# Kernel optimization log

Measured on AMD Instinct MI355X. Metric: run time of the kernel, lower is better.

Reference implementation:

```python
import jax, jax.numpy as jnp
import numpy as np

RADII = (0.4, 0.8, 1.2)
SIGMA2 = 2.0 * 0.2 ** 2   # Gaussian shell-density bandwidth
ALPHA = 0.3               # keras LeakyReLU default
EPS = 1e-3                # keras BatchNormalization default epsilon


def _n_coeffs(L):
    return sum((2 * l + 1) ** 2 for l in range(L + 1))


def _pullback_idx(L):
    # flat index of Wigner block entry (m, n=0) for each SH coeff (l, m)
    idx, off = [], 0
    for l in range(L + 1):
        d = 2 * l + 1
        idx += [off + m * d + l for m in range(d)]
        off += d * d
    return np.asarray(idx, dtype=np.int32)


def setup_inputs() -> dict:
    key = jax.random.key(0)
    ks = jax.random.split(key, 20)
    B, N, Q, S = 64, 2048, 1024, 512
    T = [_n_coeffs(l) for l in (5, 4, 3)]  # 286, 165, 84
    f32 = jnp.float32

    def nrm(k, shape, scale=1.0):
        return jax.random.normal(ks[k], shape, dtype=f32) * scale

    dirs = nrm(1, (3, S, 3))
    dirs = dirs / jnp.linalg.norm(dirs, axis=-1, keepdims=True)
    z = lambda n: jnp.zeros((n,), f32)
    o = lambda n: jnp.ones((n,), f32)
    return {
        "x": nrm(0, (B, N, 3)),
        "shell_dirs": dirs,                                   # [3, 512, 3]
        "A_sh": nrm(2, (36, S), 1.0 / np.sqrt(S)),            # SH projection (l_max=5)
        "D_eval0": nrm(3, (Q, T[0]), 1.0 / np.sqrt(T[0])),    # Wigner eval bases
        "D_eval1": nrm(4, (Q, T[1]), 1.0 / np.sqrt(T[1])),
        "D_eval2": nrm(5, (Q, T[2]), 1.0 / np.sqrt(T[2])),
        "D_coef1": nrm(6, (T[1], Q), 1.0 / np.sqrt(Q)),       # Wigner coeff (projection) bases
        "D_coef2": nrm(7, (T[2], Q), 1.0 / np.sqrt(Q)),
        "D_coef_last": nrm(8, (T[2], Q), 1.0 / np.sqrt(Q)),
        "W0": nrm(9, (3, 16), 1.0 / np.sqrt(3)), "b0": z(16),
        "W1": nrm(10, (16, 32), 0.25), "b1": z(32),
        "W2": nrm(11, (32, 64), 1.0 / np.sqrt(32)), "b2": z(64),
        "g0": o(16), "be0": z(16),
        "g1": o(32), "be1": z(32),
        "g2": o(64), "be2": z(64),
        "Wfc1": nrm(12, (256, 512), 1.0 / 16.0), "bfc1": z(512),
        "gfc1": o(512), "befc1": z(512),
        "Wfc2": nrm(13, (512, 256), 1.0 / np.sqrt(512)), "bfc2": z(256),
        "gfc2": o(256), "befc2": z(256),
        "Wout": nrm(14, (256, 40), 1.0 / 16.0), "bout": z(40),
    }


def _bn(y, g, b, axes):
    m = jnp.mean(y, axis=axes, keepdims=True)
    v = jnp.var(y, axis=axes, keepdims=True)
    return (y - m) * jax.lax.rsqrt(v + EPS) * g + b


def reference(x, shell_dirs, A_sh, D_eval0, D_eval1, D_eval2,
              D_coef1, D_coef2, D_coef_last,
              W0, b0, W1, b1, W2, b2,
              g0, be0, g1, be1, g2, be2,
              Wfc1, bfc1, gfc1, befc1, Wfc2, bfc2, gfc2, befc2,
              Wout, bout):
    B = x.shape[0]
    # --- sphere_shell_embedding: Gaussian shell density -> SH coeffs per shell ---
    xn2 = jnp.sum(x * x, -1)[..., None]                 # [B,N,1]
    sh = []
    for i, r in enumerate(RADII):
        c = r * shell_dirs[i]                           # [S,3]
        d2 = xn2 + jnp.sum(c * c, -1) - 2.0 * (x @ c.T)  # [B,N,S]
        f = jnp.mean(jnp.exp(-d2 / SIGMA2), axis=1)      # [B,S]
        sh.append(f @ A_sh.T)                            # [B,36]
    sh = jnp.stack(sh, axis=-1)                          # [B,36,3] shells as channels
    # --- S2_to_SO3_pullback: Y_lm -> D^l_{m,0} column of Wigner blocks ---
    idx = jnp.asarray(_pullback_idx(5))
    y = jnp.zeros((B, 286, 3), sh.dtype).at[:, idx, :].set(sh)
    # --- layer 0: SO3Conv (per-coeff channel mix) + WignerEval + BN + LReLU + WignerCoeffs ---
    y = jnp.einsum('btc,cu->btu', y, W0) + b0
    y = jnp.einsum('qt,btu->bqu', D_eval0, y)            # [B,1024,16]
    y = jax.nn.leaky_relu(_bn(y, g0, be0, (0, 1)), ALPHA)
    y = jnp.einsum('tq,bqu->btu', D_coef1, y)            # [B,165,16]
    # --- layer 1 ---
    y = jnp.einsum('btc,cu->btu', y, W1) + b1
    y = jnp.einsum('qt,btu->bqu', D_eval1, y)            # [B,1024,32]
    y = jax.nn.leaky_relu(_bn(y, g1, be1, (0, 1)), ALPHA)
    y = jnp.einsum('tq,bqu->btu', D_coef2, y)            # [B,84,32]
    # --- layer 2 ---
    y = jnp.einsum('btc,cu->btu', y, W2) + b2
    y = jnp.einsum('qt,btu->bqu', D_eval2, y)            # [B,1024,64]
    y = jax.nn.leaky_relu(_bn(y, g2, be2, (0, 1)), ALPHA)
    y = jnp.einsum('tq,bqu->btu', D_coef_last, y)        # [B,84,64]
    # --- degree-wise norms (rotation-invariant pooling), l_max=3 blocks ---
    offs, sizes = (0, 1, 10, 35), (1, 9, 25, 49)
    feats = jnp.concatenate(
        [jnp.linalg.norm(y[:, o:o + s, :], axis=1, keepdims=True)
         for o, s in zip(offs, sizes)], axis=1)          # [B,4,64]
    h = feats.reshape(B, -1)                             # [B,256]
    # --- MLP head (dropout = identity at inference) ---
    h = jax.nn.relu(_bn(h @ Wfc1 + bfc1, gfc1, befc1, (0,)))
    h = jax.nn.relu(_bn(h @ Wfc2 + bfc2, gfc2, befc2, (0,)))
    return jax.nn.softmax(h @ Wout + bout, axis=-1)
```

## Files before the change

### kernel.cpp

```cpp
#include <hip/hip_runtime.h>
#include <hip/hip_bf16.h>

#define BB 64
#define NN 2048
#define QQ 1024
#define SS 512
#define NCH 16
#define PREPB 609
#define QKN3 4

__device__ const int PIDX[36] = {
    0, 2, 5, 8, 12, 17, 22, 27, 32, 38, 45, 52, 59, 66, 73, 80,
    88, 97, 106, 115, 124, 133, 142, 151, 160,
    170, 181, 192, 203, 214, 225, 236, 247, 258, 269, 280};

__global__ __launch_bounds__(256) void k_preshell(
    const float* __restrict__ De0, const float* __restrict__ De1, const float* __restrict__ De2,
    float* __restrict__ Dg0t, float* __restrict__ rs0,
    float* __restrict__ Det1, float* __restrict__ Det2,
    float* __restrict__ stats,
    const float* __restrict__ x, const float* __restrict__ dirs, float* __restrict__ pbuf) {
    __shared__ float tile[32][33];
    __shared__ float4 lx[NN / NCH];
    int blk = blockIdx.x, tid = threadIdx.x;
    if (blk < PREPB) {
        int r = tid >> 5, c = tid & 31;
        if (blk < 192) {
            int tq = blk & 31, tt = blk >> 5;
            int q0 = tq * 32, t0 = tt * 32;
            for (int rr = r; rr < 32; rr += 8) {
                int t = t0 + c;
                tile[rr][c] = (t < 165) ? De1[(q0 + rr) * 165 + t] : 0.f;
            }
            __syncthreads();
            for (int rr = r; rr < 32; rr += 8) {
                int t = t0 + rr;
                if (t < 165) Det1[t * QQ + q0 + c] = tile[c][rr];
            }
        } else if (blk < 288) {
            int i = blk - 192;
            int tq = i & 31, tt = i >> 5;
            int q0 = tq * 32, t0 = tt * 32;
            for (int rr = r; rr < 32; rr += 8) {
                int t = t0 + c;
                tile[rr][c] = (t < 84) ? De2[(q0 + rr) * 84 + t] : 0.f;
            }
            __syncthreads();
            for (int rr = r; rr < 32; rr += 8) {
                int t = t0 + rr;
                if (t < 84) Det2[t * QQ + q0 + c] = tile[c][rr];
            }
        } else if (blk < 352) {
            int i = blk - 288;
            int tq = i & 31, tj = i >> 5;
            int q0 = tq * 32, j0 = tj * 32;
            for (int rr = r; rr < 32; rr += 8) {
                int j = j0 + c;
                tile[rr][c] = (j < 36) ? De0[(q0 + rr) * 286 + PIDX[j]] : 0.f;
            }
            __syncthreads();
            for (int rr = r; rr < 32; rr += 8) {
                int j = j0 + rr;
                if (j < 36) Dg0t[j * QQ + q0 + c] = tile[c][rr];
            }
        } else if (blk < 608) {
            int w = tid >> 6, lane = tid & 63;
            int q = (blk - 352) * 4 + w;
            float s = 0.f;
#pragma unroll
            for (int p = 0; p < 5; p++) {
                int idx = lane + p * 64;
                if (idx < 286) s += De0[q * 286 + idx];
            }
#pragma unroll
            for (int o = 32; o > 0; o >>= 1) s += __shfl_xor(s, o, 64);
            if (lane == 0) rs0[q] = s;
        } else {
            if (tid < 224) stats[tid] = 0.f;
        }
        return;
    }
    int idx = blk - PREPB;
    int b = idx & 63, zc = idx >> 6;
    const float KL = 18.033688011112042f;
    const float* xb = x + ((size_t)b * NN + zc * (NN / NCH)) * 3;
    for (int n = tid; n < NN / NCH; n += 256) {
        float X = xb[n * 3 + 0];
        float Y = xb[n * 3 + 1];
        float Z = xb[n * 3 + 2];
        lx[n] = make_float4(X, Y, Z, -KL * (X * X + Y * Y + Z * Z));
    }
    __syncthreads();
    float cxs[3][2], cys[3][2], czs[3][2], bas[3][2];
#pragma unroll
    for (int i = 0; i < 3; i++) {
        float r = (i == 0) ? 0.4f : ((i == 1) ? 0.8f : 1.2f);
#pragma unroll
        for (int h = 0; h < 2; h++) {
            int s = tid + h * 256;
            float cx = r * dirs[(i * SS + s) * 3 + 0];
            float cy = r * dirs[(i * SS + s) * 3 + 1];
            float cz = r * dirs[(i * SS + s) * 3 + 2];
            bas[i][h] = -KL * (cx * cx + cy * cy + cz * cz);
            cxs[i][h] = 2.f * KL * cx;
            cys[i][h] = 2.f * KL * cy;
            czs[i][h] = 2.f * KL * cz;
        }
    }
    float acc[3][2];
#pragma unroll
    for (int i = 0; i < 3; i++) { acc[i][0] = 0.f; acc[i][1] = 0.f; }
#pragma unroll 4
    for (int n = 0; n < NN / NCH; n++) {
        float4 p = lx[n];
#pragma unroll
        for (int i = 0; i < 3; i++)
#pragma unroll
            for (int h = 0; h < 2; h++)
                acc[i][h] += __builtin_amdgcn_exp2f(
                    fmaf(cxs[i][h], p.x, fmaf(cys[i][h], p.y, fmaf(czs[i][h], p.z, p.w + bas[i][h]))));
    }
#pragma unroll
    for (int i = 0; i < 3; i++) {
        float* o = pbuf + ((size_t)(zc * 3 + i) * BB + b) * SS;
        o[tid] = acc[i][0];
        o[tid + 256] = acc[i][1];
    }
}

__global__ __launch_bounds__(256) void k_eval0(const float* __restrict__ pbuf,
                                               const float* __restrict__ A_sh,
                                               const float* __restrict__ W0,
                                               const float* __restrict__ b0,
                                               const float* __restrict__ Dg0t,
                                               const float* __restrict__ rs0,
                                               float* __restrict__ yq, float* __restrict__ stats) {
    __shared__ float lf[3][SS];
    __shared__ float lsh[36][3];
    __shared__ float llm[576];
    __shared__ float lred[4][32];
    int qc = blockIdx.x, b = blockIdx.y, tid = threadIdx.x;
    for (int i = tid; i < 3 * SS; i += 256) {
        int c = i / SS, s = i % SS;
        float v = 0.f;
#pragma unroll
        for (int zc = 0; zc < NCH; zc++) v += pbuf[((size_t)(zc * 3 + c) * BB + b) * SS + s];
        lf[c][s] = v * (1.0f / NN);
    }
    __syncthreads();
    int w = tid >> 6, lane = tid & 63;
    for (int p = w; p < 108; p += 4) {
        int j = p / 3, c = p % 3;
        const float* As = A_sh + j * SS;
        float a = 0.f;
#pragma unroll
        for (int k = 0; k < 8; k++) a = fmaf(lf[c][lane + 64 * k], As[lane + 64 * k], a);
#pragma unroll
        for (int o = 32; o > 0; o >>= 1) a += __shfl_xor(a, o, 64);
        if (lane == 0) lsh[j][c] = a;
    }
    __syncthreads();
    for (int i = tid; i < 576; i += 256) {
        int j = i >> 4, u = i & 15;
        float m = 0.f;
#pragma unroll
        for (int c = 0; c < 3; c++) m = fmaf(lsh[j][c], W0[c * 16 + u], m);
        llm[i] = m;
    }
    __syncthreads();
    int q = qc * 256 + tid;
    float acc[16];
#pragma unroll
    for (int u = 0; u < 16; u++) acc[u] = 0.f;
#pragma unroll 4
    for (int j = 0; j < 36; j++) {
        float d = Dg0t[j * QQ + q];
#pragma unroll
        for (int u = 0; u < 16; u++) acc[u] = fmaf(d, llm[j * 16 + u], acc[u]);
    }
    float rb = rs0[q];
#pragma unroll
    for (int u = 0; u < 16; u++) acc[u] = fmaf(b0[u], rb, acc[u]);
#pragma unroll
    for (int u = 0; u < 16; u++) yq[((size_t)b * 16 + u) * QQ + q] = acc[u];
#pragma unroll
    for (int u = 0; u < 16; u++) {
        float v = acc[u], v2 = acc[u] * acc[u];
#pragma unroll
        for (int o = 32; o > 0; o >>= 1) {
            v += __shfl_xor(v, o, 64);
            v2 += __shfl_xor(v2, o, 64);
        }
        if (lane == 0) { lred[w][u] = v; lred[w][16 + u] = v2; }
    }
    __syncthreads();
    if (tid < 32) atomicAdd(&stats[tid], lred[0][tid] + lred[1][tid] + lred[2][tid] + lred[3][tid]);
}

template <int TT, int UU, int QKN>
__global__ __launch_bounds__(256) void k_coefG(const float* __restrict__ yq,
                                               const float* __restrict__ Dc,
                                               const float* __restrict__ stats,
                                               const float* __restrict__ g,
                                               const float* __restrict__ be,
                                               float* __restrict__ part) {
    constexpr int KC = QQ / QKN;
    __shared__ float lA[32][68];
    __shared__ float lB[32][68];
    __shared__ float lsu[UU], ltu[UU];
    int mt = blockIdx.x, nt = blockIdx.y, qk = blockIdx.z, tid = threadIdx.x;
    int m0 = mt * 64, n0 = nt * 64, k0 = qk * KC;
    if (tid < UU) {
        const float inv = 1.0f / (BB * QQ);
        float mm = stats[tid] * inv;
        float var = stats[UU + tid] * inv - mm * mm;
        float s = g[tid] * rsqrtf(fmaxf(var, 0.f) + 1e-3f);
        lsu[tid] = s;
        ltu[tid] = be[tid] - mm * s;
    }
    __syncthreads();
    int r = tid >> 2;
    int f = (tid & 3) * 4;
    bool mok = (m0 + r) < TT;
    const float* arow = Dc + (size_t)(mok ? (m0 + r) : 0) * QQ;
    const float* brow = yq + (size_t)(n0 + r) * QQ;
    float su = lsu[(n0 + r) % UU], tu = ltu[(n0 + r) % UU];
    int tg = tid >> 4, ug = tid & 15;
    float acc[4][4];
#pragma unroll
    for (int i = 0; i < 4; i++)
#pragma unroll
        for (int j = 0; j < 4; j++) acc[i][j] = 0.f;
    for (int kb = 0; kb < KC; kb += 32) {
        int kg = k0 + kb;
#pragma unroll
        for (int p = 0; p < 2; p++) {
            int ko = f + p * 16;
            float4 a4 = make_float4(0.f, 0.f, 0.f, 0.f);
            if (mok) a4 = *(const float4*)(arow + kg + ko);
            float4 b4 = *(const float4*)(brow + kg + ko);
#pragma unroll
            for (int i = 0; i < 4; i++) {
                float v = fmaf((&b4.x)[i], su, tu);
                lA[ko + i][r] = (&a4.x)[i];
                lB[ko + i][r] = (v > 0.f) ? v : 0.3f * v;
            }
        }
        __syncthreads();
#pragma unroll 2
        for (int kk = 0; kk < 32; kk++) {
            float4 a4 = *(const float4*)&lA[kk][tg * 4];
            float4 b4 = *(const float4*)&lB[kk][ug * 4];
#pragma unroll
            for (int i = 0; i < 4; i++) {
                float av = (&a4.x)[i];
                acc[i][0] = fmaf(av, b4.x, acc[i][0]);
                acc[i][1] = fmaf(av, b4.y, acc[i][1]);
                acc[i][2] = fmaf(av, b4.z, acc[i][2]);
                acc[i][3] = fmaf(av, b4.w, acc[i][3]);
            }
        }
        __syncthreads();
    }
    int n = n0 + ug * 4;
    int b = n / UU, u0 = n % UU;
#pragma unroll
    for (int i = 0; i < 4; i++) {
        int t = m0 + tg * 4 + i;
        if (t < TT)
            *(float4*)&part[(((size_t)qk * BB + b) * TT + t) * UU + u0] =
                make_float4(acc[i][0], acc[i][1], acc[i][2], acc[i][3]);
    }
}

template <int TT, int CC, int UU, int QKN>
__global__ __launch_bounds__(256) void k_eval(const float* __restrict__ part,
                                              const float* __restrict__ W, const float* __restrict__ bias,
                                              const float* __restrict__ Det,
                                              float* __restrict__ yq, float* __restrict__ stats) {
    __shared__ float lyt[TT * CC];
    __shared__ float lym[TT * 16];
    __shared__ float lred[4][32];
    int qc = blockIdx.x, b = blockIdx.y, uz = blockIdx.z * 16, tid = threadIdx.x;
    for (int i = tid; i < TT * CC; i += 256) {
        float v = 0.f;
#pragma unroll
        for (int k = 0; k < QKN; k++) v += part[(size_t)k * (BB * TT * CC) + (size_t)b * TT * CC + i];
        lyt[i] = v;
    }
    __syncthreads();
    for (int e = tid; e < TT * 16; e += 256) {
        int t = e >> 4, ul = e & 15, u = uz + ul;
        float m = bias[u];
#pragma unroll
        for (int c = 0; c < CC; c++) m = fmaf(lyt[t * CC + c], W[c * UU + u], m);
        lym[e] = m;
    }
    __syncthreads();
    int q = qc * 256 + tid;
    float acc[16];
#pragma unroll
    for (int u = 0; u < 16; u++) acc[u] = 0.f;
#pragma unroll 4
    for (int t = 0; t < TT; t++) {
        float d = Det[t * QQ + q];
#pragma unroll
        for (int u = 0; u < 16; u++) acc[u] = fmaf(d, lym[t * 16 + u], acc[u]);
    }
#pragma unroll
    for (int u = 0; u < 16; u++) yq[((size_t)b * UU + uz + u) * QQ + q] = acc[u];
    int lane = tid & 63, w = tid >> 6;
#pragma unroll
    for (int u = 0; u < 16; u++) {
        float v = acc[u], v2 = acc[u] * acc[u];
#pragma unroll
        for (int o = 32; o > 0; o >>= 1) {
            v += __shfl_xor(v, o, 64);
            v2 += __shfl_xor(v2, o, 64);
        }
        if (lane == 0) { lred[w][u] = v; lred[w][16 + u] = v2; }
    }
    __syncthreads();
    if (tid < 32) {
        float s = lred[0][tid] + lred[1][tid] + lred[2][tid] + lred[3][tid];
        int idx = (tid < 16) ? (uz + tid) : (UU + uz + tid - 16);
        atomicAdd(&stats[idx], s);
    }
}

__global__ __launch_bounds__(256) void k_norms(const float* __restrict__ part, float* __restrict__ ht0) {
    __shared__ float ly[84 * 64];
    int b = blockIdx.x, tid = threadIdx.x;
    for (int i = tid; i < 84 * 64; i += 256) {
        float v = 0.f;
#pragma unroll
        for (int k = 0; k < QKN3; k++) v += part[(size_t)k * (BB * 84 * 64) + b * (84 * 64) + i];
        ly[i] = v;
    }
    __syncthreads();
    int blk = tid >> 6, u = tid & 63;
    const int offs[4] = {0, 1, 10, 35};
    const int ends[4] = {1, 10, 35, 84};
    float a = 0.f;
    for (int t = offs[blk]; t < ends[blk]; t++) {
        float v = ly[t * 64 + u];
        a = fmaf(v, v, a);
    }
    ht0[(blk * 64 + u) * BB + b] = sqrtf(fmaxf(a, 0.f));
}

template <int K, int J>
__global__ __launch_bounds__(512) void k_fc(const float* __restrict__ in, const float* __restrict__ W,
                                            const float* __restrict__ bias, const float* __restrict__ g,
                                            const float* __restrict__ be, float* __restrict__ out) {
    __shared__ float red[8][64];
    int j = blockIdx.x;
    int b = threadIdx.x & 63, kq = threadIdx.x >> 6;
    constexpr int KS = K / 8;
    int kbeg = kq * KS;
    float a0 = 0.f, a1 = 0.f, a2 = 0.f, a3 = 0.f;
#pragma unroll 4
    for (int k = kbeg; k < kbeg + KS; k += 4) {
        a0 = fmaf(in[k * BB + b], W[(size_t)k * J + j], a0);
        a1 = fmaf(in[(k + 1) * BB + b], W[(size_t)(k + 1) * J + j], a1);
        a2 = fmaf(in[(k + 2) * BB + b], W[(size_t)(k + 2) * J + j], a2);
        a3 = fmaf(in[(k + 3) * BB + b], W[(size_t)(k + 3) * J + j], a3);
    }
    red[kq][b] = (a0 + a1) + (a2 + a3);
    __syncthreads();
    if (kq == 0) {
        float acc = bias[j];
#pragma unroll
        for (int i = 0; i < 8; i++) acc += red[i][b];
        float s1 = acc, s2 = acc * acc;
#pragma unroll
        for (int o = 32; o > 0; o >>= 1) {
            s1 += __shfl_xor(s1, o, 64);
            s2 += __shfl_xor(s2, o, 64);
        }
        float m = s1 * (1.0f / 64.f);
        float var = s2 * (1.0f / 64.f) - m * m;
        float sc = g[j] * rsqrtf(fmaxf(var, 0.f) + 1e-3f);
        float v = (acc - m) * sc + be[j];
        out[j * BB + b] = fmaxf(v, 0.f);
    }
}

__global__ __launch_bounds__(256) void k_out(const float* __restrict__ ht2, const float* __restrict__ Wout,
                                             const float* __restrict__ bout, float* __restrict__ outp) {
    __shared__ float red[4][64];
    __shared__ float sm[64];
    int b = blockIdx.x;
    int o = threadIdx.x & 63, kq = threadIdx.x >> 6;
    float a0 = 0.f, a1 = 0.f, a2 = 0.f, a3 = 0.f;
    int kbeg = kq * 64;
    if (o < 40) {
#pragma unroll 4
        for (int k = kbeg; k < kbeg + 64; k += 4) {
            a0 = fmaf(ht2[k * BB + b], Wout[k * 40 + o], a0);
            a1 = fmaf(ht2[(k + 1) * BB + b], Wout[(k + 1) * 40 + o], a1);
            a2 = fmaf(ht2[(k + 2) * BB + b], Wout[(k + 2) * 40 + o], a2);
            a3 = fmaf(ht2[(k + 3) * BB + b], Wout[(k + 3) * 40 + o], a3);
        }
    }
    red[kq][o] = (a0 + a1) + (a2 + a3);
    __syncthreads();
    if (kq == 0) {
        float acc = red[0][o] + red[1][o] + red[2][o] + red[3][o] + ((o < 40) ? bout[o] : 0.f);
        sm[o] = (o < 40) ? acc : -3.0e38f;
        __syncthreads();
        for (int s = 32; s > 0; s >>= 1) {
            if (o < s) sm[o] = fmaxf(sm[o], sm[o + s]);
            __syncthreads();
        }
        float m = sm[0];
        __syncthreads();
        const float L2E = 1.4426950408889634f;
        float e = (o < 40) ? exp2f((acc - m) * L2E) : 0.f;
        sm[o] = e;
        __syncthreads();
        for (int s = 32; s > 0; s >>= 1) {
            if (o < s) sm[o] += sm[o + s];
            __syncthreads();
        }
        if (o < 40) outp[b * 40 + o] = e / sm[0];
    }
}

#define OFF_PBUF 0
#define OFF_DG0T 1572864
#define OFF_RS0 1609728
#define OFF_DET1 1610752
#define OFF_DET2 1779712
#define OFF_YQ 1865728
#define OFF_HT0 6060032
#define OFF_HT1 6076416
#define OFF_HT2 6109184
#define OFF_STATS 6125568

extern "C" void kernel_launch(void* const* d_in, const int* in_sizes, int n_in,
                              void* d_out, int out_size, void* d_ws, size_t ws_size,
                              hipStream_t stream) {
    const float* x = (const float*)d_in[0];
    const float* shell_dirs = (const float*)d_in[1];
    const float* A_sh = (const float*)d_in[2];
    const float* D_eval0 = (const float*)d_in[3];
    const float* D_eval1 = (const float*)d_in[4];
    const float* D_eval2 = (const float*)d_in[5];
    const float* D_coef1 = (const float*)d_in[6];
    const float* D_coef2 = (const float*)d_in[7];
    const float* D_coef_last = (const float*)d_in[8];
    const float* W0 = (const float*)d_in[9];
    const float* b0 = (const float*)d_in[10];
    const float* W1 = (const float*)d_in[11];
    const float* b1 = (const float*)d_in[12];
    const float* W2 = (const float*)d_in[13];
    const float* b2 = (const float*)d_in[14];
    const float* g0 = (const float*)d_in[15];
    const float* be0 = (const float*)d_in[16];
    const float* g1 = (const float*)d_in[17];
    const float* be1 = (const float*)d_in[18];
    const float* g2 = (const float*)d_in[19];
    const float* be2 = (const float*)d_in[20];
    const float* Wfc1 = (const float*)d_in[21];
    const float* bfc1 = (const float*)d_in[22];
    const float* gfc1 = (const float*)d_in[23];
    const float* befc1 = (const float*)d_in[24];
    const float* Wfc2 = (const float*)d_in[25];
    const float* bfc2 = (const float*)d_in[26];
    const float* gfc2 = (const float*)d_in[27];
    const float* befc2 = (const float*)d_in[28];
    const float* Wout = (const float*)d_in[29];
    const float* bout = (const float*)d_in[30];
    float* out = (float*)d_out;

    float* ws = (float*)d_ws;
    float* pbuf = ws + OFF_PBUF;
    float* part = ws + OFF_PBUF;
    float* Dg0t = ws + OFF_DG0T;
    float* rs0 = ws + OFF_RS0;
    float* Det1 = ws + OFF_DET1;
    float* Det2 = ws + OFF_DET2;
    float* yq = ws + OFF_YQ;
    float* ht0 = ws + OFF_HT0;
    float* ht1 = ws + OFF_HT1;
    float* ht2 = ws + OFF_HT2;
    float* stats = ws + OFF_STATS;
    float* stats0 = stats;
    float* stats1 = stats + 32;
    float* stats2 = stats + 96;

    k_preshell<<<PREPB + BB * NCH, 256, 0, stream>>>(
        D_eval0, D_eval1, D_eval2, Dg0t, rs0, Det1, Det2, stats, x, shell_dirs, pbuf);
    k_eval0<<<dim3(4, BB), 256, 0, stream>>>(pbuf, A_sh, W0, b0, Dg0t, rs0, yq, stats0);
    k_coefG<165, 16, 8><<<dim3(3, 16, 8), 256, 0, stream>>>(yq, D_coef1, stats0, g0, be0, part);
    k_eval<165, 16, 32, 8><<<dim3(4, BB, 2), 256, 0, stream>>>(part, W1, b1, Det1, yq, stats1);
    k_coefG<84, 32, 8><<<dim3(2, 32, 8), 256, 0, stream>>>(yq, D_coef2, stats1, g1, be1, part);
    k_eval<84, 32, 64, 8><<<dim3(4, BB, 4), 256, 0, stream>>>(part, W2, b2, Det2, yq, stats2);
    k_coefG<84, 64, QKN3><<<dim3(2, 64, QKN3), 256, 0, stream>>>(yq, D_coef_last, stats2, g2, be2, part);
    k_norms<<<BB, 256, 0, stream>>>(part, ht0);
    k_fc<256, 512><<<512, 512, 0, stream>>>(ht0, Wfc1, bfc1, gfc1, befc1, ht1);
    k_fc<512, 256><<<256, 512, 0, stream>>>(ht1, Wfc2, bfc2, gfc2, befc2, ht2);
    k_out<<<BB, 256, 0, stream>>>(ht2, Wout, bout, out);
}
```

Before: 345.7 us.

## Split eval into channel-mix kernel plus register-tiled GEMM for Wigner evaluation

Replaces the fused k_eval (partial reduction, channel mix and Det evaluation in one kernel) with two kernels. k_redmix reduces the split-K partials and applies W plus bias into a padded [B*U, TTp] matrix. k_evalG then runs a 64x64 shared-memory tiled GEMM with 4x4 register blocking against Det, fusing the BN statistics reduction. The old kernel redid the channel mix in every block and read lym from LDS once per FMA. The new version gains reuse but adds a launch and a round trip of the ym intermediate through global memory.

```diff
diff --git a/kernel.cpp b/kernel.cpp
--- a/kernel.cpp
+++ b/kernel.cpp
@@ -273,58 +273,112 @@
     }
 }
 
-template <int TT, int CC, int UU, int QKN>
-__global__ __launch_bounds__(256) void k_eval(const float* __restrict__ part,
-                                              const float* __restrict__ W, const float* __restrict__ bias,
-                                              const float* __restrict__ Det,
-                                              float* __restrict__ yq, float* __restrict__ stats) {
-    __shared__ float lyt[TT * CC];
-    __shared__ float lym[TT * 16];
-    __shared__ float lred[4][32];
-    int qc = blockIdx.x, b = blockIdx.y, uz = blockIdx.z * 16, tid = threadIdx.x;
+template <int TT, int CC, int UU, int QKN, int TTp>
+__global__ __launch_bounds__(256) void k_redmix(const float* __restrict__ part,
+                                                const float* __restrict__ W,
+                                                const float* __restrict__ bias,
+                                                float* __restrict__ ym) {
+    constexpr int CCp = CC + 1;
+    __shared__ float lyt[TT * CCp];
+    int b = blockIdx.x, tid = threadIdx.x;
     for (int i = tid; i < TT * CC; i += 256) {
         float v = 0.f;
 #pragma unroll
         for (int k = 0; k < QKN; k++) v += part[(size_t)k * (BB * TT * CC) + (size_t)b * TT * CC + i];
-        lyt[i] = v;
-    }
-    __syncthreads();
-    for (int e = tid; e < TT * 16; e += 256) {
-        int t = e >> 4, ul = e & 15, u = uz + ul;
-        float m = bias[u];
-#pragma unroll
-        for (int c = 0; c < CC; c++) m = fmaf(lyt[t * CC + c], W[c * UU + u], m);
-        lym[e] = m;
-    }
-    __syncthreads();
-    int q = qc * 256 + tid;
-    float acc[16];
-#pragma unroll
-    for (int u = 0; u < 16; u++) acc[u] = 0.f;
-#pragma unroll 4
-    for (int t = 0; t < TT; t++) {
-        float d = Det[t * QQ + q];
-#pragma unroll
-        for (int u = 0; u < 16; u++) acc[u] = fmaf(d, lym[t * 16 + u], acc[u]);
-    }
-#pragma unroll
-    for (int u = 0; u < 16; u++) yq[((size_t)b * UU + uz + u) * QQ + q] = acc[u];
-    int lane = tid & 63, w = tid >> 6;
-#pragma unroll
-    for (int u = 0; u < 16; u++) {
-        float v = acc[u], v2 = acc[u] * acc[u];
-#pragma unroll
-        for (int o = 32; o > 0; o >>= 1) {
-            v += __shfl_xor(v, o, 64);
-            v2 += __shfl_xor(v2, o, 64);
-        }
-        if (lane == 0) { lred[w][u] = v; lred[w][16 + u] = v2; }
-    }
-    __syncthreads();
-    if (tid < 32) {
-        float s = lred[0][tid] + lred[1][tid] + lred[2][tid] + lred[3][tid];
-        int idx = (tid < 16) ? (uz + tid) : (UU + uz + tid - 16);
-        atomicAdd(&stats[idx], s);
+        lyt[(i / CC) * CCp + (i % CC)] = v;
+    }
+    __syncthreads();
+    for (int i = tid; i < UU * TTp; i += 256) {
+        int u = i / TTp, t = i % TTp;
+        float m = 0.f;
+        if (t < TT) {
+            m = bias[u];
+#pragma unroll
+            for (int c = 0; c < CC; c++) m = fmaf(lyt[t * CCp + c], W[c * UU + u], m);
+        }
+        ym[((size_t)b * UU + u) * TTp + t] = m;
+    }
+}
+
+template <int TT, int TTp, int UU>
+__global__ __launch_bounds__(256) void k_evalG(const float* __restrict__ ym,
+                                               const float* __restrict__ Det,
+                                               float* __restrict__ yq,
+                                               float* __restrict__ stats) {
+    __shared__ float lA[32][68];
+    __shared__ float lB[32][68];
+    __shared__ float sred[2][64];
+    int mt = blockIdx.x, qt = blockIdx.y, tid = threadIdx.x;
+    int m0 = mt * 64, q0 = qt * 64;
+    int r = tid >> 2, f = (tid & 3) * 4;
+    const float* arow = ym + (size_t)(m0 + r) * TTp;
+    int br = tid >> 4, bq = (tid & 15) * 4;
+    int tg = tid >> 4, ug = tid & 15;
+    float acc[4][4];
+#pragma unroll
+    for (int i = 0; i < 4; i++)
+#pragma unroll
+        for (int j = 0; j < 4; j++) acc[i][j] = 0.f;
+    for (int kb = 0; kb < TT; kb += 32) {
+#pragma unroll
+        for (int p = 0; p < 2; p++) {
+            int ko = f + p * 16;
+            float4 a4 = *(const float4*)(arow + kb + ko);
+#pragma unroll
+            for (int i = 0; i < 4; i++) lA[ko + i][r] = (&a4.x)[i];
+            int kk = br + p * 16;
+            int t = kb + kk;
+            float4 b4 = make_float4(0.f, 0.f, 0.f, 0.f);
+            if (t < TT) b4 = *(const float4*)(Det + (size_t)t * QQ + q0 + bq);
+            *(float4*)&lB[kk][bq] = b4;
+        }
+        __syncthreads();
+#pragma unroll 2
+        for (int kk = 0; kk < 32; kk++) {
+            float4 a4 = *(const float4*)&lA[kk][tg * 4];
+            float4 b4 = *(const float4*)&lB[kk][ug * 4];
+#pragma unroll
+            for (int i = 0; i < 4; i++) {
+                float av = (&a4.x)[i];
+                acc[i][0] = fmaf(av, b4.x, acc[i][0]);
+                acc[i][1] = fmaf(av, b4.y, acc[i][1]);
+                acc[i][2] = fmaf(av, b4.z, acc[i][2]);
+                acc[i][3] = fmaf(av, b4.w, acc[i][3]);
+            }
+        }
+        __syncthreads();
+    }
+    float s1[4], s2[4];
+#pragma unroll
+    for (int i = 0; i < 4; i++) {
+        int m = m0 + tg * 4 + i;
+        *(float4*)&yq[(size_t)m * QQ + q0 + ug * 4] =
+            make_float4(acc[i][0], acc[i][1], acc[i][2], acc[i][3]);
+        s1[i] = (acc[i][0] + acc[i][1]) + (acc[i][2] + acc[i][3]);
+        s2[i] = fmaf(acc[i][0], acc[i][0], fmaf(acc[i][1], acc[i][1],
+                 fmaf(acc[i][2], acc[i][2], acc[i][3] * acc[i][3])));
+    }
+#pragma unroll
+    for (int o = 1; o < 16; o <<= 1) {
+#pragma unroll
+        for (int i = 0; i < 4; i++) {
+            s1[i] += __shfl_xor(s1[i], o, 64);
+            s2[i] += __shfl_xor(s2[i], o, 64);
+        }
+    }
+    if (ug == 0) {
+#pragma unroll
+        for (int i = 0; i < 4; i++) {
+            sred[0][tg * 4 + i] = s1[i];
+            sred[1][tg * 4 + i] = s2[i];
+        }
+    }
+    __syncthreads();
+    if (tid < 2 * UU) {
+        int which = tid / UU, u = tid % UU;
+        float s = 0.f;
+        for (int rr = u; rr < 64; rr += UU) s += sred[which][rr];
+        atomicAdd(&stats[which * UU + u], s);
     }
 }
 
@@ -433,10 +487,11 @@
 #define OFF_DET1 1610752
 #define OFF_DET2 1779712
 #define OFF_YQ 1865728
-#define OFF_HT0 6060032
-#define OFF_HT1 6076416
-#define OFF_HT2 6109184
-#define OFF_STATS 6125568
+#define OFF_YM 6060032
+#define OFF_HT0 6453248
+#define OFF_HT1 6469632
+#define OFF_HT2 6502400
+#define OFF_STATS 6518784
 
 extern "C" void kernel_launch(void* const* d_in, const int* in_sizes, int n_in,
                               void* d_out, int out_size, void* d_ws, size_t ws_size,
@@ -482,6 +537,7 @@
     float* Det1 = ws + OFF_DET1;
     float* Det2 = ws + OFF_DET2;
     float* yq = ws + OFF_YQ;
+    float* ym = ws + OFF_YM;
     float* ht0 = ws + OFF_HT0;
     float* ht1 = ws + OFF_HT1;
     float* ht2 = ws + OFF_HT2;
@@ -494,9 +550,11 @@
         D_eval0, D_eval1, D_eval2, Dg0t, rs0, Det1, Det2, stats, x, shell_dirs, pbuf);
     k_eval0<<<dim3(4, BB), 256, 0, stream>>>(pbuf, A_sh, W0, b0, Dg0t, rs0, yq, stats0);
     k_coefG<165, 16, 8><<<dim3(3, 16, 8), 256, 0, stream>>>(yq, D_coef1, stats0, g0, be0, part);
-    k_eval<165, 16, 32, 8><<<dim3(4, BB, 2), 256, 0, stream>>>(part, W1, b1, Det1, yq, stats1);
+    k_redmix<165, 16, 32, 8, 192><<<BB, 256, 0, stream>>>(part, W1, b1, ym);
+    k_evalG<165, 192, 32><<<dim3(32, 16), 256, 0, stream>>>(ym, Det1, yq, stats1);
     k_coefG<84, 32, 8><<<dim3(2, 32, 8), 256, 0, stream>>>(yq, D_coef2, stats1, g1, be1, part);
-    k_eval<84, 32, 64, 8><<<dim3(4, BB, 4), 256, 0, stream>>>(part, W2, b2, Det2, yq, stats2);
+    k_redmix<84, 32, 64, 8, 96><<<BB, 256, 0, stream>>>(part, W2, b2, ym);
+    k_evalG<84, 96, 64><<<dim3(64, 16), 256, 0, stream>>>(ym, Det2, yq, stats2);
     k_coefG<84, 64, QKN3><<<dim3(2, 64, QKN3), 256, 0, stream>>>(yq, D_coef_last, stats2, g2, be2, part);
     k_norms<<<BB, 256, 0, stream>>>(part, ht0);
     k_fc<256, 512><<<512, 512, 0, stream>>>(ht0, Wfc1, bfc1, gfc1, befc1, ht1);
```

New measurement: 353.5 us. +2.3%, slower.
